# Performance work log

Measured on AMD Instinct MI355X. Metric: run time of the kernel, lower is better.

The kernel has to match this reference:

```python
import jax, jax.numpy as jnp
import numpy as np

EMBED_DIM = 1024
NUM_HEADS = 16
HEAD_DIM = EMBED_DIM // NUM_HEADS
SCALE = HEAD_DIM ** -0.5


def setup_inputs() -> dict:
    key = jax.random.key(0)
    ks = jax.random.split(key, 5)
    B, N, C = 4, 2048, EMBED_DIM
    s = C ** -0.5
    return {
        "x": jax.random.normal(ks[0], (B, N, C), dtype=jnp.float32),
        "w_qkv": jax.random.normal(ks[1], (C, 3 * C), dtype=jnp.float32) * s,
        "b_qkv": jnp.zeros((3 * C,), dtype=jnp.float32),
        "w_proj": jax.random.normal(ks[2], (C, C), dtype=jnp.float32) * s,
        "b_proj": jnp.zeros((C,), dtype=jnp.float32),
    }


def reference(x, w_qkv, b_qkv, w_proj, b_proj):
    B, N, C = x.shape
    H, D = NUM_HEADS, HEAD_DIM
    qkv = x @ w_qkv + b_qkv                      # (B, N, 3C)
    qkv = qkv.reshape(B, N, 3, H, D)
    qkv = jnp.transpose(qkv, (2, 0, 3, 1, 4))    # (3, B, H, N, D)
    q, k, v = qkv[0], qkv[1], qkv[2]
    attn = jnp.einsum('bhnd,bhmd->bhnm', q, k) * SCALE
    attn = jax.nn.softmax(attn, axis=-1)
    out = jnp.einsum('bhnm,bhmd->bhnd', attn, v)  # (B, H, N, D)
    out = jnp.transpose(out, (0, 2, 1, 3)).reshape(B, N, C)
    return out @ w_proj + b_proj
```

## Files before the change

### kernel.cpp

```cpp
#include <hip/hip_runtime.h>

typedef __attribute__((ext_vector_type(8))) short short8v;
typedef __attribute__((ext_vector_type(4))) short short4v;
typedef __attribute__((ext_vector_type(4))) float float4v;
typedef __attribute__((ext_vector_type(4))) unsigned short ushort4v;
typedef __attribute__((ext_vector_type(8))) unsigned short ushort8v;

#define GLOBAL_AS __attribute__((address_space(1)))
#define LDS_AS __attribute__((address_space(3)))

__device__ __forceinline__ void async_cp16(const void* g, void* l) {
  __builtin_amdgcn_global_load_lds((const GLOBAL_AS void*)g, (LDS_AS void*)l, 16, 0, 0);
}

__device__ __forceinline__ unsigned short f2bf(float f) {
  unsigned u = __float_as_uint(f);
  u += 0x7fffu + ((u >> 16) & 1u);
  return (unsigned short)(u >> 16);
}

#if defined(__HIP_DEVICE_COMPILE__)
#if __has_builtin(__builtin_amdgcn_exp2f)
#define EXP2F(x) __builtin_amdgcn_exp2f(x)
#else
#define EXP2F(x) exp2f(x)
#endif
#else
#define EXP2F(x) exp2f(x)
#endif

#if defined(__HIP_DEVICE_COMPILE__) && __has_builtin(__builtin_amdgcn_cvt_pk_bf16_f32)
typedef __attribute__((ext_vector_type(2))) __bf16 bf16x2v;
__device__ __forceinline__ unsigned pk_bf16(float a, float b) {
  bf16x2v r = __builtin_amdgcn_cvt_pk_bf16_f32(a, b);
  return __builtin_bit_cast(unsigned, r);
}
#else
__device__ __forceinline__ unsigned pk_bf16(float a, float b) {
  return (unsigned)f2bf(a) | ((unsigned)f2bf(b) << 16);
}
#endif

#define MFMA_QK(a, b, c) __builtin_amdgcn_mfma_f32_16x16x32_bf16(a, b, c, 0, 0, 0)


__global__ __launch_bounds__(256) void cvt_f32_bf16(const float* __restrict__ src,
                                                    unsigned short* __restrict__ dst) {
  int i = blockIdx.x * 256 + threadIdx.x;
  float4 v = ((const float4*)src)[i];
  ushort4v o;
  o.x = f2bf(v.x); o.y = f2bf(v.y); o.z = f2bf(v.z); o.w = f2bf(v.w);
  ((ushort4v*)dst)[i] = o;
}

__global__ __launch_bounds__(256) void transpose_w(const float* __restrict__ src,
                                                   unsigned short* __restrict__ dst,
                                                   int K, int N) {
  __shared__ float tile[64][65];
  int k0 = blockIdx.x * 64, n0 = blockIdx.y * 64;
  int t = threadIdx.x;
  int tc = t & 15, tr = t >> 4;
#pragma unroll
  for (int p = 0; p < 4; p++) {
    int r = tr + p * 16;
    float4 v = *(const float4*)(src + (size_t)(k0 + r) * N + n0 + tc * 4);
    tile[r][tc * 4 + 0] = v.x; tile[r][tc * 4 + 1] = v.y;
    tile[r][tc * 4 + 2] = v.z; tile[r][tc * 4 + 3] = v.w;
  }
  __syncthreads();
#pragma unroll
  for (int p = 0; p < 4; p++) {
    int rn = tr + p * 16;
    ushort4v o;
    o.x = f2bf(tile[tc * 4 + 0][rn]);
    o.y = f2bf(tile[tc * 4 + 1][rn]);
    o.z = f2bf(tile[tc * 4 + 2][rn]);
    o.w = f2bf(tile[tc * 4 + 3][rn]);
    *(ushort4v*)(dst + (size_t)(n0 + rn) * K + k0 + tc * 4) = o;
  }
}


__global__ __launch_bounds__(256) void gemm_qkv(const unsigned short* __restrict__ A,
                                                const unsigned short* __restrict__ BT,
                                                const float* __restrict__ bias,
                                                unsigned short* __restrict__ Qo,
                                                unsigned short* __restrict__ Ko,
                                                unsigned short* __restrict__ VTo) {
  __shared__ unsigned short As[128 * 32];
  __shared__ unsigned short Bs[128 * 32];
  int tid = threadIdx.x;
  int lane = tid & 63, w = tid >> 6, g = lane >> 4, c = lane & 15;
  int m0 = blockIdx.x * 128, n0 = blockIdx.y * 128;
  int wm = (w & 1) * 64, wn = (w >> 1) * 64;
  float4v acc[4][4] = {};

  for (int k0 = 0; k0 < 1024; k0 += 32) {
    __syncthreads();
#pragma unroll
    for (int p = 0; p < 2; p++) {
      int idx = p * 256 + tid;
      int row = idx >> 2, c8 = (idx & 3) * 8;
      async_cp16(A + (size_t)(m0 + row) * 1024 + k0 + c8, &As[idx * 8]);
      async_cp16(BT + (size_t)(n0 + row) * 1024 + k0 + c8, &Bs[idx * 8]);
    }
    __syncthreads();
    short8v af[4], bf[4];
#pragma unroll
    for (int i = 0; i < 4; i++)
      af[i] = *(const short8v*)(&As[(wm + i * 16 + c) * 32 + g * 8]);
#pragma unroll
    for (int j = 0; j < 4; j++)
      bf[j] = *(const short8v*)(&Bs[(wn + j * 16 + c) * 32 + g * 8]);
#pragma unroll
    for (int i = 0; i < 4; i++)
#pragma unroll
      for (int j = 0; j < 4; j++)
        acc[i][j] = MFMA_QK(af[i], bf[j], acc[i][j]);
  }

  int which = n0 >> 10;
#pragma unroll
  for (int j = 0; j < 4; j++) {
    int ng = n0 + wn + j * 16 + c;
    float bv = bias[ng];
    int h = (ng & 1023) >> 6, d = ng & 63;
#pragma unroll
    for (int i = 0; i < 4; i++) {
#pragma unroll
      for (int r = 0; r < 4; r++) {
        int mg = m0 + wm + i * 16 + g * 4 + r;
        int b = mg >> 11, n = mg & 2047;
        float v = acc[i][j][r] + bv;
        if (which == 0)
          Qo[((size_t)(b * 16 + h) * 2048 + n) * 64 + d] = f2bf(v * 0.18033688011112042f);
        else if (which == 1)
          Ko[((size_t)(b * 16 + h) * 2048 + n) * 64 + d] = f2bf(v);
        else {
          int np = (n & ~31) | (((n >> 2) & 3) << 3) | (((n >> 4) & 1) << 2) | (n & 3);
          VTo[((size_t)(b * 16 + h) * 64 + d) * 2048 + np] = f2bf(v);
        }
      }
    }
  }
}


#define NTOK 2048
#define BK 64

__global__ __launch_bounds__(256, 2) void attn_kernel(const unsigned short* __restrict__ Qg,
                                                      const unsigned short* __restrict__ Kg,
                                                      const unsigned short* __restrict__ VTg,
                                                      unsigned short* __restrict__ Og) {
  __shared__ unsigned short Ks[2][BK * 64];
  __shared__ unsigned short VTs[2][64 * BK];

  int tid = threadIdx.x;
  int lane = tid & 63, w = tid >> 6, g = lane >> 4, c = lane & 15;
  int id = blockIdx.x;
  int xcd = id & 7, within = id >> 3;
  int bh = xcd * 8 + (within >> 3);
  int q0 = (within & 7) * 256;

  const unsigned short* Qb = Qg + (size_t)bh * NTOK * 64;
  const unsigned short* Kb = Kg + (size_t)bh * NTOK * 64;
  const unsigned short* VTb = VTg + (size_t)bh * 64 * NTOK;

  short8v qf[4][2];
#pragma unroll
  for (int nt = 0; nt < 4; nt++)
#pragma unroll
    for (int kk = 0; kk < 2; kk++)
      qf[nt][kk] = *(const short8v*)(Qb + (size_t)(q0 + w * 64 + nt * 16 + c) * 64 +
                                     kk * 32 + g * 8);

  short8v ones8;
#pragma unroll
  for (int i = 0; i < 8; i++) ones8[i] = (short)0x3F80;

  float4v lacc[4] = {};
  float4v o[4][4] = {};

#pragma unroll
  for (int p = 0; p < 2; p++) {
    int idx = p * 256 + tid;
    int row = idx >> 3, ch = idx & 7;
    async_cp16(Kb + (size_t)row * 64 + ((ch ^ (row & 7)) * 8), &Ks[0][idx * 8]);
    async_cp16(VTb + (size_t)row * NTOK + ((ch ^ (row & 7)) * 8), &VTs[0][idx * 8]);
  }

  for (int it = 0; it < NTOK / BK; it++) {
    int pb = it & 1;
    __syncthreads();

    if (it + 1 < NTOK / BK) {
      int kt = (it + 1) * BK;
#pragma unroll
      for (int p = 0; p < 2; p++) {
        int idx = p * 256 + tid;
        int row = idx >> 3, ch = idx & 7;
        async_cp16(Kb + (size_t)(kt + row) * 64 + ((ch ^ (row & 7)) * 8),
                   &Ks[1 - pb][idx * 8]);
        async_cp16(VTb + (size_t)row * NTOK + kt + ((ch ^ (row & 7)) * 8),
                   &VTs[1 - pb][idx * 8]);
      }
    }

    const unsigned short* Kp = &Ks[pb][0];
    const unsigned short* Vp = &VTs[pb][0];

#pragma unroll
    for (int t = 0; t < 2; t++) {
      float4v st[2][4] = {};
      __builtin_amdgcn_s_setprio(1);
#pragma unroll
      for (int mth = 0; mth < 2; mth++) {
        int row = (t * 2 + mth) * 16 + c;
        short8v kf[2];
#pragma unroll
        for (int kk = 0; kk < 2; kk++) {
          int ch = (kk * 4 + g) ^ (row & 7);
          kf[kk] = *(const short8v*)(Kp + row * 64 + ch * 8);
        }
#pragma unroll
        for (int nt = 0; nt < 4; nt++)
#pragma unroll
          for (int kk = 0; kk < 2; kk++)
            st[mth][nt] = MFMA_QK(kf[kk], qf[nt][kk], st[mth][nt]);
      }
      __builtin_amdgcn_s_setprio(0);

      short8v pa8[4];
#pragma unroll
      for (int nt = 0; nt < 4; nt++) {
        float4v a = st[0][nt], b2 = st[1][nt];
        a.x = EXP2F(a.x); a.y = EXP2F(a.y); a.z = EXP2F(a.z); a.w = EXP2F(a.w);
        b2.x = EXP2F(b2.x); b2.y = EXP2F(b2.y); b2.z = EXP2F(b2.z); b2.w = EXP2F(b2.w);
        union { unsigned u[4]; short8v s; } cv;
        cv.u[0] = pk_bf16(a.x, a.y);
        cv.u[1] = pk_bf16(a.z, a.w);
        cv.u[2] = pk_bf16(b2.x, b2.y);
        cv.u[3] = pk_bf16(b2.z, b2.w);
        pa8[nt] = cv.s;
      }

      __builtin_amdgcn_s_setprio(1);
#pragma unroll
      for (int nt_o = 0; nt_o < 4; nt_o++) {
        int d = nt_o * 16 + c;
        int s = (t * 4 + g) ^ (d & 7);
        short8v vb8 = *(const short8v*)(Vp + d * BK + s * 8);
#pragma unroll
        for (int mt = 0; mt < 4; mt++)
          o[mt][nt_o] = MFMA_QK(pa8[mt], vb8, o[mt][nt_o]);
      }
#pragma unroll
      for (int mt = 0; mt < 4; mt++)
        lacc[mt] = MFMA_QK(pa8[mt], ones8, lacc[mt]);
      __builtin_amdgcn_s_setprio(0);
    }
  }

  int b = bh >> 4, h = bh & 15;
#pragma unroll
  for (int mt = 0; mt < 4; mt++) {
    float4v li;
#pragma unroll
    for (int r = 0; r < 4; r++) li[r] = 1.0f / lacc[mt][r];
#pragma unroll
    for (int nt_o = 0; nt_o < 4; nt_o++) {
      float4v v = o[mt][nt_o] * li;
      int col = h * 64 + nt_o * 16 + c;
      int rowbase = b * NTOK + q0 + w * 64 + mt * 16 + g * 4;
#pragma unroll
      for (int r = 0; r < 4; r++)
        Og[(size_t)(rowbase + r) * 1024 + col] = f2bf(v[r]);
    }
  }
}

__global__ __launch_bounds__(256) void gemm_proj(const unsigned short* __restrict__ A,
                                                 const unsigned short* __restrict__ BT,
                                                 const float* __restrict__ bias,
                                                 float* __restrict__ out) {
  __shared__ unsigned short As[128 * 32];
  __shared__ unsigned short Bs[128 * 32];
  int tid = threadIdx.x;
  int lane = tid & 63, w = tid >> 6, g = lane >> 4, c = lane & 15;
  int m0 = blockIdx.x * 128, n0 = blockIdx.y * 128;
  int wm = (w & 1) * 64, wn = (w >> 1) * 64;
  float4v acc[4][4] = {};

  for (int k0 = 0; k0 < 1024; k0 += 32) {
    __syncthreads();
#pragma unroll
    for (int p = 0; p < 2; p++) {
      int idx = p * 256 + tid;
      int row = idx >> 2, c8 = (idx & 3) * 8;
      async_cp16(A + (size_t)(m0 + row) * 1024 + k0 + c8, &As[idx * 8]);
      async_cp16(BT + (size_t)(n0 + row) * 1024 + k0 + c8, &Bs[idx * 8]);
    }
    __syncthreads();
    short8v af[4], bf[4];
#pragma unroll
    for (int i = 0; i < 4; i++)
      af[i] = *(const short8v*)(&As[(wm + i * 16 + c) * 32 + g * 8]);
#pragma unroll
    for (int j = 0; j < 4; j++)
      bf[j] = *(const short8v*)(&Bs[(wn + j * 16 + c) * 32 + g * 8]);
#pragma unroll
    for (int i = 0; i < 4; i++)
#pragma unroll
      for (int j = 0; j < 4; j++)
        acc[i][j] = MFMA_QK(af[i], bf[j], acc[i][j]);
  }

#pragma unroll
  for (int j = 0; j < 4; j++) {
    int ng = n0 + wn + j * 16 + c;
    float bv = bias[ng];
#pragma unroll
    for (int i = 0; i < 4; i++) {
#pragma unroll
      for (int r = 0; r < 4; r++) {
        int mg = m0 + wm + i * 16 + g * 4 + r;
        out[(size_t)mg * 1024 + ng] = acc[i][j][r] + bv;
      }
    }
  }
}


extern "C" void kernel_launch(void* const* d_in, const int* in_sizes, int n_in,
                              void* d_out, int out_size, void* d_ws, size_t ws_size,
                              hipStream_t stream) {
  (void)in_sizes; (void)n_in; (void)out_size; (void)ws_size;
  const float* x = (const float*)d_in[0];
  const float* w_qkv = (const float*)d_in[1];
  const float* b_qkv = (const float*)d_in[2];
  const float* w_proj = (const float*)d_in[3];
  const float* b_proj = (const float*)d_in[4];
  float* out = (float*)d_out;

  unsigned short* x_bf = (unsigned short*)d_ws;
  unsigned short* wqkvT = x_bf + (size_t)8192 * 1024;
  unsigned short* wprojT = wqkvT + (size_t)3072 * 1024;
  unsigned short* qws = wprojT + (size_t)1024 * 1024;
  unsigned short* kws = qws + (size_t)8388608;
  unsigned short* vtws = kws + (size_t)8388608;
  unsigned short* aws = vtws + (size_t)8388608;

  cvt_f32_bf16<<<8192, 256, 0, stream>>>(x, x_bf);
  transpose_w<<<dim3(16, 48), 256, 0, stream>>>(w_qkv, wqkvT, 1024, 3072);
  transpose_w<<<dim3(16, 16), 256, 0, stream>>>(w_proj, wprojT, 1024, 1024);
  gemm_qkv<<<dim3(64, 24), 256, 0, stream>>>(x_bf, wqkvT, b_qkv, qws, kws, vtws);
  attn_kernel<<<512, 256, 0, stream>>>(qws, kws, vtws, aws);
  gemm_proj<<<dim3(64, 8), 256, 0, stream>>>(aws, wprojT, b_proj, out);
}
```

Baseline: 294.9 us.

## Double-buffer LDS tiles with XOR swizzle in QKV and projection GEMMs

Both GEMM kernels now keep two LDS buffers. The async global-to-LDS copy for the next K-slice is issued before the MFMA work on the current slice, which drops the second barrier per iteration and overlaps load latency with compute. The 16-byte chunk placement in LDS is XOR-swizzled by row to reduce bank conflicts on the short8 fragment reads. Launch bounds now request 4 blocks per CU, which doubles LDS per block and may constrain register allocation.

```diff
diff --git a/kernel.cpp b/kernel.cpp
--- a/kernel.cpp
+++ b/kernel.cpp
@@ -81,37 +81,54 @@
 }
 
 
-__global__ __launch_bounds__(256) void gemm_qkv(const unsigned short* __restrict__ A,
-                                                const unsigned short* __restrict__ BT,
-                                                const float* __restrict__ bias,
-                                                unsigned short* __restrict__ Qo,
-                                                unsigned short* __restrict__ Ko,
-                                                unsigned short* __restrict__ VTo) {
-  __shared__ unsigned short As[128 * 32];
-  __shared__ unsigned short Bs[128 * 32];
+__device__ __forceinline__ void stage128x32(const unsigned short* __restrict__ A,
+                                            const unsigned short* __restrict__ BT,
+                                            unsigned short* as, unsigned short* bs,
+                                            int m0, int n0, int k0, int tid) {
+#pragma unroll
+  for (int p = 0; p < 2; p++) {
+    int idx = p * 256 + tid;
+    int row = idx >> 2, s = idx & 3;
+    int ch = s ^ ((row >> 1) & 3);
+    async_cp16(A + (size_t)(m0 + row) * 1024 + k0 + ch * 8, as + idx * 8);
+    async_cp16(BT + (size_t)(n0 + row) * 1024 + k0 + ch * 8, bs + idx * 8);
+  }
+}
+
+
+__global__ __launch_bounds__(256, 4) void gemm_qkv(const unsigned short* __restrict__ A,
+                                                   const unsigned short* __restrict__ BT,
+                                                   const float* __restrict__ bias,
+                                                   unsigned short* __restrict__ Qo,
+                                                   unsigned short* __restrict__ Ko,
+                                                   unsigned short* __restrict__ VTo) {
+  __shared__ unsigned short As[2][128 * 32];
+  __shared__ unsigned short Bs[2][128 * 32];
   int tid = threadIdx.x;
   int lane = tid & 63, w = tid >> 6, g = lane >> 4, c = lane & 15;
   int m0 = blockIdx.x * 128, n0 = blockIdx.y * 128;
   int wm = (w & 1) * 64, wn = (w >> 1) * 64;
   float4v acc[4][4] = {};
 
-  for (int k0 = 0; k0 < 1024; k0 += 32) {
+  stage128x32(A, BT, &As[0][0], &Bs[0][0], m0, n0, 0, tid);
+
+  for (int it = 0; it < 32; ++it) {
+    int pb = it & 1;
     __syncthreads();
-#pragma unroll
-    for (int p = 0; p < 2; p++) {
-      int idx = p * 256 + tid;
-      int row = idx >> 2, c8 = (idx & 3) * 8;
-      async_cp16(A + (size_t)(m0 + row) * 1024 + k0 + c8, &As[idx * 8]);
-      async_cp16(BT + (size_t)(n0 + row) * 1024 + k0 + c8, &Bs[idx * 8]);
-    }
-    __syncthreads();
+    if (it + 1 < 32)
+      stage128x32(A, BT, &As[1 - pb][0], &Bs[1 - pb][0], m0, n0, (it + 1) * 32, tid);
+
     short8v af[4], bf[4];
 #pragma unroll
-    for (int i = 0; i < 4; i++)
-      af[i] = *(const short8v*)(&As[(wm + i * 16 + c) * 32 + g * 8]);
-#pragma unroll
-    for (int j = 0; j < 4; j++)
-      bf[j] = *(const short8v*)(&Bs[(wn + j * 16 + c) * 32 + g * 8]);
+    for (int i = 0; i < 4; i++) {
+      int r = wm + i * 16 + c;
+      af[i] = *(const short8v*)(&As[pb][r * 32 + (g ^ ((r >> 1) & 3)) * 8]);
+    }
+#pragma unroll
+    for (int j = 0; j < 4; j++) {
+      int r = wn + j * 16 + c;
+      bf[j] = *(const short8v*)(&Bs[pb][r * 32 + (g ^ ((r >> 1) & 3)) * 8]);
+    }
 #pragma unroll
     for (int i = 0; i < 4; i++)
 #pragma unroll
@@ -280,35 +297,37 @@
   }
 }
 
-__global__ __launch_bounds__(256) void gemm_proj(const unsigned short* __restrict__ A,
-                                                 const unsigned short* __restrict__ BT,
-                                                 const float* __restrict__ bias,
-                                                 float* __restrict__ out) {
-  __shared__ unsigned short As[128 * 32];
-  __shared__ unsigned short Bs[128 * 32];
+__global__ __launch_bounds__(256, 4) void gemm_proj(const unsigned short* __restrict__ A,
+                                                    const unsigned short* __restrict__ BT,
+                                                    const float* __restrict__ bias,
+                                                    float* __restrict__ out) {
+  __shared__ unsigned short As[2][128 * 32];
+  __shared__ unsigned short Bs[2][128 * 32];
   int tid = threadIdx.x;
   int lane = tid & 63, w = tid >> 6, g = lane >> 4, c = lane & 15;
   int m0 = blockIdx.x * 128, n0 = blockIdx.y * 128;
   int wm = (w & 1) * 64, wn = (w >> 1) * 64;
   float4v acc[4][4] = {};
 
-  for (int k0 = 0; k0 < 1024; k0 += 32) {
+  stage128x32(A, BT, &As[0][0], &Bs[0][0], m0, n0, 0, tid);
+
+  for (int it = 0; it < 32; ++it) {
+    int pb = it & 1;
     __syncthreads();
-#pragma unroll
-    for (int p = 0; p < 2; p++) {
-      int idx = p * 256 + tid;
-      int row = idx >> 2, c8 = (idx & 3) * 8;
-      async_cp16(A + (size_t)(m0 + row) * 1024 + k0 + c8, &As[idx * 8]);
-      async_cp16(BT + (size_t)(n0 + row) * 1024 + k0 + c8, &Bs[idx * 8]);
-    }
-    __syncthreads();
+    if (it + 1 < 32)
+      stage128x32(A, BT, &As[1 - pb][0], &Bs[1 - pb][0], m0, n0, (it + 1) * 32, tid);
+
     short8v af[4], bf[4];
 #pragma unroll
-    for (int i = 0; i < 4; i++)
-      af[i] = *(const short8v*)(&As[(wm + i * 16 + c) * 32 + g * 8]);
-#pragma unroll
-    for (int j = 0; j < 4; j++)
-      bf[j] = *(const short8v*)(&Bs[(wn + j * 16 + c) * 32 + g * 8]);
+    for (int i = 0; i < 4; i++) {
+      int r = wm + i * 16 + c;
+      af[i] = *(const short8v*)(&As[pb][r * 32 + (g ^ ((r >> 1) & 3)) * 8]);
+    }
+#pragma unroll
+    for (int j = 0; j < 4; j++) {
+      int r = wn + j * 16 + c;
+      bf[j] = *(const short8v*)(&Bs[pb][r * 32 + (g ^ ((r >> 1) & 3)) * 8]);
+    }
 #pragma unroll
     for (int i = 0; i < 4; i++)
 #pragma unroll
```

Result: faster. 287.9 us (-2.4%).

## Rewrite QKV and projection GEMMs with larger tiles and triple-buffered async pipeline

Applied to the files above, without the earlier changes.

Both GEMMs now use 512-thread blocks with larger tiles (256x256 for QKV, 128x256 for projection). K-slices are triple-buffered through LDS with async global-to-LDS copies issued two steps ahead and gated by explicit vmcnt waits and raw barriers. LDS chunks are XOR-swizzled to avoid bank conflicts, MFMA phases are wrapped in s_setprio, and block IDs are remapped for L2 locality. This aims to hide global load latency and raise data reuse, in exchange for higher register and LDS pressure and fragile hand-written wait counts.

```diff
diff --git a/kernel.cpp b/kernel.cpp
--- a/kernel.cpp
+++ b/kernel.cpp
@@ -43,6 +43,12 @@
 
 #define MFMA_QK(a, b, c) __builtin_amdgcn_mfma_f32_16x16x32_bf16(a, b, c, 0, 0, 0)
 
+__device__ __forceinline__ void wg_barrier() {
+  asm volatile("" ::: "memory");
+  __builtin_amdgcn_s_barrier();
+  asm volatile("" ::: "memory");
+}
+
 
 __global__ __launch_bounds__(256) void cvt_f32_bf16(const float* __restrict__ src,
                                                     unsigned short* __restrict__ dst) {
@@ -81,55 +87,110 @@
 }
 
 
-__global__ __launch_bounds__(256) void gemm_qkv(const unsigned short* __restrict__ A,
-                                                const unsigned short* __restrict__ BT,
-                                                const float* __restrict__ bias,
-                                                unsigned short* __restrict__ Qo,
-                                                unsigned short* __restrict__ Ko,
-                                                unsigned short* __restrict__ VTo) {
-  __shared__ unsigned short As[128 * 32];
-  __shared__ unsigned short Bs[128 * 32];
+__device__ __forceinline__ void stage256x32(const unsigned short* __restrict__ src,
+                                            unsigned short* dst, int r0, int k0, int tid) {
+#pragma unroll
+  for (int p = 0; p < 2; p++) {
+    int idx = p * 512 + tid;
+    int row = idx >> 2, s = idx & 3;
+    int ch = s ^ ((row >> 1) & 3);
+    async_cp16(src + (size_t)(r0 + row) * 1024 + k0 + ch * 8, dst + idx * 8);
+  }
+}
+
+__device__ __forceinline__ void stage128x32(const unsigned short* __restrict__ src,
+                                            unsigned short* dst, int r0, int k0, int tid) {
+  int row = tid >> 2, s = tid & 3;
+  int ch = s ^ ((row >> 1) & 3);
+  async_cp16(src + (size_t)(r0 + row) * 1024 + k0 + ch * 8, dst + tid * 8);
+}
+
+
+__global__ __launch_bounds__(512, 2) void gemm_qkv(const unsigned short* __restrict__ A,
+                                                   const unsigned short* __restrict__ BT,
+                                                   const float* __restrict__ bias,
+                                                   unsigned short* __restrict__ Qo,
+                                                   unsigned short* __restrict__ Ko,
+                                                   unsigned short* __restrict__ VTo) {
+  __shared__ unsigned short As[3][256 * 32];
+  __shared__ unsigned short Bs[3][256 * 32];
   int tid = threadIdx.x;
-  int lane = tid & 63, w = tid >> 6, g = lane >> 4, c = lane & 15;
-  int m0 = blockIdx.x * 128, n0 = blockIdx.y * 128;
-  int wm = (w & 1) * 64, wn = (w >> 1) * 64;
-  float4v acc[4][4] = {};
-
-  for (int k0 = 0; k0 < 1024; k0 += 32) {
-    __syncthreads();
-#pragma unroll
-    for (int p = 0; p < 2; p++) {
-      int idx = p * 256 + tid;
-      int row = idx >> 2, c8 = (idx & 3) * 8;
-      async_cp16(A + (size_t)(m0 + row) * 1024 + k0 + c8, &As[idx * 8]);
-      async_cp16(BT + (size_t)(n0 + row) * 1024 + k0 + c8, &Bs[idx * 8]);
-    }
-    __syncthreads();
-    short8v af[4], bf[4];
-#pragma unroll
-    for (int i = 0; i < 4; i++)
-      af[i] = *(const short8v*)(&As[(wm + i * 16 + c) * 32 + g * 8]);
-#pragma unroll
-    for (int j = 0; j < 4; j++)
-      bf[j] = *(const short8v*)(&Bs[(wn + j * 16 + c) * 32 + g * 8]);
+  int lane = tid & 63, w = tid >> 6, g = (lane >> 4) & 3, c = lane & 15;
+  int wr = w >> 2, wc = w & 3;
+  int id = blockIdx.x;
+  int swz = (id & 7) * 48 + (id >> 3);
+  int m0 = (swz & 31) * 256, n0 = (swz >> 5) * 256;
+
+  float4v acc[8][4] = {};
+  short8v bf[4];
+
+  stage256x32(A, &As[0][0], m0, 0, tid);
+  stage256x32(BT, &Bs[0][0], n0, 0, tid);
+  stage256x32(A, &As[1][0], m0, 32, tid);
+  stage256x32(BT, &Bs[1][0], n0, 32, tid);
+  asm volatile("s_waitcnt vmcnt(4)" ::: "memory");
+  wg_barrier();
+
+  int cb = 0;
+  for (int t = 0; t < 32; ++t) {
+    int nb = cb + 2; if (nb >= 3) nb -= 3;
+    const unsigned short* Ap = &As[cb][0];
+    const unsigned short* Bp = &Bs[cb][0];
+
+    short8v af[4];
+#pragma unroll
+    for (int i = 0; i < 4; i++) {
+      int r = wr * 128 + i * 16 + c;
+      af[i] = *(const short8v*)(Ap + r * 32 + (g ^ ((r >> 1) & 3)) * 8);
+    }
+#pragma unroll
+    for (int j = 0; j < 4; j++) {
+      int r = wc * 64 + j * 16 + c;
+      bf[j] = *(const short8v*)(Bp + r * 32 + (g ^ ((r >> 1) & 3)) * 8);
+    }
+    if (t + 2 < 32) stage256x32(A, &As[nb][0], m0, (t + 2) * 32, tid);
+    wg_barrier();
+    __builtin_amdgcn_s_setprio(1);
 #pragma unroll
     for (int i = 0; i < 4; i++)
 #pragma unroll
       for (int j = 0; j < 4; j++)
         acc[i][j] = MFMA_QK(af[i], bf[j], acc[i][j]);
+    __builtin_amdgcn_s_setprio(0);
+    wg_barrier();
+
+#pragma unroll
+    for (int i = 0; i < 4; i++) {
+      int r = wr * 128 + 64 + i * 16 + c;
+      af[i] = *(const short8v*)(Ap + r * 32 + (g ^ ((r >> 1) & 3)) * 8);
+    }
+    if (t + 2 < 32) stage256x32(BT, &Bs[nb][0], n0, (t + 2) * 32, tid);
+    if (t < 30) { asm volatile("s_waitcnt vmcnt(4)" ::: "memory"); }
+    else        { asm volatile("s_waitcnt vmcnt(0)" ::: "memory"); }
+    wg_barrier();
+    __builtin_amdgcn_s_setprio(1);
+#pragma unroll
+    for (int i = 0; i < 4; i++)
+#pragma unroll
+      for (int j = 0; j < 4; j++)
+        acc[4 + i][j] = MFMA_QK(af[i], bf[j], acc[4 + i][j]);
+    __builtin_amdgcn_s_setprio(0);
+    wg_barrier();
+
+    cb = cb + 1 == 3 ? 0 : cb + 1;
   }
 
   int which = n0 >> 10;
 #pragma unroll
   for (int j = 0; j < 4; j++) {
-    int ng = n0 + wn + j * 16 + c;
+    int ng = n0 + wc * 64 + j * 16 + c;
     float bv = bias[ng];
     int h = (ng & 1023) >> 6, d = ng & 63;
 #pragma unroll
-    for (int i = 0; i < 4; i++) {
+    for (int i = 0; i < 8; i++) {
 #pragma unroll
       for (int r = 0; r < 4; r++) {
-        int mg = m0 + wm + i * 16 + g * 4 + r;
+        int mg = m0 + wr * 128 + i * 16 + g * 4 + r;
         int b = mg >> 11, n = mg & 2047;
         float v = acc[i][j][r] + bv;
         if (which == 0)
@@ -280,51 +341,88 @@
   }
 }
 
-__global__ __launch_bounds__(256) void gemm_proj(const unsigned short* __restrict__ A,
-                                                 const unsigned short* __restrict__ BT,
-                                                 const float* __restrict__ bias,
-                                                 float* __restrict__ out) {
-  __shared__ unsigned short As[128 * 32];
-  __shared__ unsigned short Bs[128 * 32];
+
+__global__ __launch_bounds__(512, 2) void gemm_proj(const unsigned short* __restrict__ A,
+                                                    const unsigned short* __restrict__ BT,
+                                                    const float* __restrict__ bias,
+                                                    float* __restrict__ out) {
+  __shared__ unsigned short As[3][128 * 32];
+  __shared__ unsigned short Bs[3][256 * 32];
   int tid = threadIdx.x;
-  int lane = tid & 63, w = tid >> 6, g = lane >> 4, c = lane & 15;
-  int m0 = blockIdx.x * 128, n0 = blockIdx.y * 128;
-  int wm = (w & 1) * 64, wn = (w >> 1) * 64;
+  int lane = tid & 63, w = tid >> 6, g = (lane >> 4) & 3, c = lane & 15;
+  int wr = w >> 2, wc = w & 3;
+  int id = blockIdx.x;
+  int swz = (id & 7) * 32 + (id >> 3);
+  int m0 = (swz & 63) * 128, n0 = (swz >> 6) * 256;
+
   float4v acc[4][4] = {};
-
-  for (int k0 = 0; k0 < 1024; k0 += 32) {
-    __syncthreads();
-#pragma unroll
-    for (int p = 0; p < 2; p++) {
-      int idx = p * 256 + tid;
-      int row = idx >> 2, c8 = (idx & 3) * 8;
-      async_cp16(A + (size_t)(m0 + row) * 1024 + k0 + c8, &As[idx * 8]);
-      async_cp16(BT + (size_t)(n0 + row) * 1024 + k0 + c8, &Bs[idx * 8]);
-    }
-    __syncthreads();
-    short8v af[4], bf[4];
-#pragma unroll
-    for (int i = 0; i < 4; i++)
-      af[i] = *(const short8v*)(&As[(wm + i * 16 + c) * 32 + g * 8]);
-#pragma unroll
-    for (int j = 0; j < 4; j++)
-      bf[j] = *(const short8v*)(&Bs[(wn + j * 16 + c) * 32 + g * 8]);
-#pragma unroll
-    for (int i = 0; i < 4; i++)
+  short8v bf[4];
+
+  stage128x32(A, &As[0][0], m0, 0, tid);
+  stage256x32(BT, &Bs[0][0], n0, 0, tid);
+  stage128x32(A, &As[1][0], m0, 32, tid);
+  stage256x32(BT, &Bs[1][0], n0, 32, tid);
+  asm volatile("s_waitcnt vmcnt(3)" ::: "memory");
+  wg_barrier();
+
+  int cb = 0;
+  for (int t = 0; t < 32; ++t) {
+    int nb = cb + 2; if (nb >= 3) nb -= 3;
+    const unsigned short* Ap = &As[cb][0];
+    const unsigned short* Bp = &Bs[cb][0];
+
+    short8v af[2];
+#pragma unroll
+    for (int i = 0; i < 2; i++) {
+      int r = wr * 64 + i * 16 + c;
+      af[i] = *(const short8v*)(Ap + r * 32 + (g ^ ((r >> 1) & 3)) * 8);
+    }
+#pragma unroll
+    for (int j = 0; j < 4; j++) {
+      int r = wc * 64 + j * 16 + c;
+      bf[j] = *(const short8v*)(Bp + r * 32 + (g ^ ((r >> 1) & 3)) * 8);
+    }
+    if (t + 2 < 32) stage128x32(A, &As[nb][0], m0, (t + 2) * 32, tid);
+    wg_barrier();
+    __builtin_amdgcn_s_setprio(1);
+#pragma unroll
+    for (int i = 0; i < 2; i++)
 #pragma unroll
       for (int j = 0; j < 4; j++)
         acc[i][j] = MFMA_QK(af[i], bf[j], acc[i][j]);
+    __builtin_amdgcn_s_setprio(0);
+    wg_barrier();
+
+#pragma unroll
+    for (int i = 0; i < 2; i++) {
+      int r = wr * 64 + 32 + i * 16 + c;
+      af[i] = *(const short8v*)(Ap + r * 32 + (g ^ ((r >> 1) & 3)) * 8);
+    }
+    if (t + 2 < 32) stage256x32(BT, &Bs[nb][0], n0, (t + 2) * 32, tid);
+    if (t < 30) { asm volatile("s_waitcnt vmcnt(3)" ::: "memory"); }
+    else        { asm volatile("s_waitcnt vmcnt(0)" ::: "memory"); }
+    wg_barrier();
+    __builtin_amdgcn_s_setprio(1);
+#pragma unroll
+    for (int i = 0; i < 2; i++)
+#pragma unroll
+      for (int j = 0; j < 4; j++)
+        acc[2 + i][j] = MFMA_QK(af[i], bf[j], acc[2 + i][j]);
+    __builtin_amdgcn_s_setprio(0);
+    wg_barrier();
+
+    cb = cb + 1 == 3 ? 0 : cb + 1;
   }
 
 #pragma unroll
   for (int j = 0; j < 4; j++) {
-    int ng = n0 + wn + j * 16 + c;
+    int ng = n0 + wc * 64 + j * 16 + c;
     float bv = bias[ng];
 #pragma unroll
     for (int i = 0; i < 4; i++) {
 #pragma unroll
       for (int r = 0; r < 4; r++) {
-        int mg = m0 + wm + i * 16 + g * 4 + r;
+        int mg = m0 + wr * 64 + i * 16 + g * 4 + r;
         out[(size_t)mg * 1024 + ng] = acc[i][j][r] + bv;
       }
     }
@@ -354,7 +452,7 @@
   cvt_f32_bf16<<<8192, 256, 0, stream>>>(x, x_bf);
   transpose_w<<<dim3(16, 48), 256, 0, stream>>>(w_qkv, wqkvT, 1024, 3072);
   transpose_w<<<dim3(16, 16), 256, 0, stream>>>(w_proj, wprojT, 1024, 1024);
-  gemm_qkv<<<dim3(64, 24), 256, 0, stream>>>(x_bf, wqkvT, b_qkv, qws, kws, vtws);
+  gemm_qkv<<<384, 512, 0, stream>>>(x_bf, wqkvT, b_qkv, qws, kws, vtws);
   attn_kernel<<<512, 256, 0, stream>>>(qws, kws, vtws, aws);
-  gemm_proj<<<dim3(64, 8), 256, 0, stream>>>(aws, wprojT, b_proj, out);
-}
+  gemm_proj<<<256, 512, 0, stream>>>(aws, wprojT, b_proj, out);
+}
```

New measurement: 336.6 us. 14.1% more time.

## Swizzle GEMM LDS tiles and stage V-transpose epilogue through LDS

Applied to the files above, without the earlier changes.

Applies an XOR swizzle on the 16-byte chunk index when staging A/B tiles into LDS in both the QKV and projection GEMMs, so the per-lane short8 fragment reads hit fewer bank conflicts. For the V third of the QKV GEMM, the epilogue now writes packed bf16 results into a padded LDS tile and reads them back so each lane stores 16-byte vectors along the token dimension, replacing scattered 2-byte transposed writes. This adds an extra shared-memory buffer and two barriers in the V path. It relies on a pk_bf16 helper defined outside the shown code and on the permuted token ordering matching what the attention kernel expects.

```diff
diff --git a/kernel.cpp b/kernel.cpp
--- a/kernel.cpp
+++ b/kernel.cpp
@@ -80,6 +80,19 @@
   }
 }
 
+__device__ __forceinline__ void stage128x32(const unsigned short* __restrict__ src,
+                                            unsigned short* dst, int r0, int k0, int tid) {
+#pragma unroll
+  for (int p = 0; p < 2; p++) {
+    int idx = p * 256 + tid;
+    int row = idx >> 2, s = idx & 3;
+    int ch = s ^ ((row >> 1) & 3);
+    async_cp16(src + (size_t)(r0 + row) * 1024 + k0 + ch * 8, dst + idx * 8);
+  }
+}
+
+
+#define TT_STRIDE 136
 
 __global__ __launch_bounds__(256) void gemm_qkv(const unsigned short* __restrict__ A,
                                                 const unsigned short* __restrict__ BT,
@@ -87,8 +100,9 @@
                                                 unsigned short* __restrict__ Qo,
                                                 unsigned short* __restrict__ Ko,
                                                 unsigned short* __restrict__ VTo) {
-  __shared__ unsigned short As[128 * 32];
-  __shared__ unsigned short Bs[128 * 32];
+  __shared__ unsigned short smem[128 * TT_STRIDE];
+  unsigned short* As = smem;
+  unsigned short* Bs = smem + 4096;
   int tid = threadIdx.x;
   int lane = tid & 63, w = tid >> 6, g = lane >> 4, c = lane & 15;
   int m0 = blockIdx.x * 128, n0 = blockIdx.y * 128;
@@ -97,21 +111,20 @@
 
   for (int k0 = 0; k0 < 1024; k0 += 32) {
     __syncthreads();
-#pragma unroll
-    for (int p = 0; p < 2; p++) {
-      int idx = p * 256 + tid;
-      int row = idx >> 2, c8 = (idx & 3) * 8;
-      async_cp16(A + (size_t)(m0 + row) * 1024 + k0 + c8, &As[idx * 8]);
-      async_cp16(BT + (size_t)(n0 + row) * 1024 + k0 + c8, &Bs[idx * 8]);
-    }
+    stage128x32(A, As, m0, k0, tid);
+    stage128x32(BT, Bs, n0, k0, tid);
     __syncthreads();
     short8v af[4], bf[4];
 #pragma unroll
-    for (int i = 0; i < 4; i++)
-      af[i] = *(const short8v*)(&As[(wm + i * 16 + c) * 32 + g * 8]);
-#pragma unroll
-    for (int j = 0; j < 4; j++)
-      bf[j] = *(const short8v*)(&Bs[(wn + j * 16 + c) * 32 + g * 8]);
+    for (int i = 0; i < 4; i++) {
+      int r = wm + i * 16 + c;
+      af[i] = *(const short8v*)(&As[r * 32 + (g ^ ((r >> 1) & 3)) * 8]);
+    }
+#pragma unroll
+    for (int j = 0; j < 4; j++) {
+      int r = wn + j * 16 + c;
+      bf[j] = *(const short8v*)(&Bs[r * 32 + (g ^ ((r >> 1) & 3)) * 8]);
+    }
 #pragma unroll
     for (int i = 0; i < 4; i++)
 #pragma unroll
@@ -120,27 +133,56 @@
   }
 
   int which = n0 >> 10;
-#pragma unroll
-  for (int j = 0; j < 4; j++) {
-    int ng = n0 + wn + j * 16 + c;
-    float bv = bias[ng];
-    int h = (ng & 1023) >> 6, d = ng & 63;
-#pragma unroll
-    for (int i = 0; i < 4; i++) {
-#pragma unroll
-      for (int r = 0; r < 4; r++) {
-        int mg = m0 + wm + i * 16 + g * 4 + r;
-        int b = mg >> 11, n = mg & 2047;
-        float v = acc[i][j][r] + bv;
-        if (which == 0)
-          Qo[((size_t)(b * 16 + h) * 2048 + n) * 64 + d] = f2bf(v * 0.18033688011112042f);
-        else if (which == 1)
-          Ko[((size_t)(b * 16 + h) * 2048 + n) * 64 + d] = f2bf(v);
-        else {
-          int np = (n & ~31) | (((n >> 2) & 3) << 3) | (((n >> 4) & 1) << 2) | (n & 3);
-          VTo[((size_t)(b * 16 + h) * 64 + d) * 2048 + np] = f2bf(v);
+  if (which != 2) {
+#pragma unroll
+    for (int j = 0; j < 4; j++) {
+      int ng = n0 + wn + j * 16 + c;
+      float bv = bias[ng];
+      int h = (ng & 1023) >> 6, d = ng & 63;
+#pragma unroll
+      for (int i = 0; i < 4; i++) {
+#pragma unroll
+        for (int r = 0; r < 4; r++) {
+          int mg = m0 + wm + i * 16 + g * 4 + r;
+          int b = mg >> 11, n = mg & 2047;
+          float v = acc[i][j][r] + bv;
+          if (which == 0)
+            Qo[((size_t)(b * 16 + h) * 2048 + n) * 64 + d] = f2bf(v * 0.18033688011112042f);
+          else
+            Ko[((size_t)(b * 16 + h) * 2048 + n) * 64 + d] = f2bf(v);
         }
       }
+    }
+  } else {
+    __syncthreads();
+#pragma unroll
+    for (int j = 0; j < 4; j++) {
+      int nl = wn + j * 16 + c;
+      float bv = bias[n0 + nl];
+#pragma unroll
+      for (int i = 0; i < 4; i++) {
+        int ml = wm + i * 16 + g * 4;
+        unsigned p0 = pk_bf16(acc[i][j][0] + bv, acc[i][j][1] + bv);
+        unsigned p1 = pk_bf16(acc[i][j][2] + bv, acc[i][j][3] + bv);
+        *(unsigned*)(smem + nl * TT_STRIDE + ml) = p0;
+        *(unsigned*)(smem + nl * TT_STRIDE + ml + 2) = p1;
+      }
+    }
+    __syncthreads();
+    int rr = lane >> 4, tc = lane & 15;
+    int P = tc & 3, g32 = tc >> 2;
+    int b = m0 >> 11, mloc = m0 & 2047;
+    int h0 = (n0 & 1023) >> 6;
+#pragma unroll
+    for (int s = 0; s < 8; s++) {
+      int row = w * 32 + s * 4 + rr;
+      int h = h0 + (row >> 6), d = row & 63;
+      const unsigned short* bp = smem + row * TT_STRIDE + g32 * 32 + P * 4;
+      union { unsigned long long q[2]; ushort8v v; } u;
+      u.q[0] = *(const unsigned long long*)(bp);
+      u.q[1] = *(const unsigned long long*)(bp + 16);
+      size_t gaddr = ((size_t)(b * 16 + h) * 64 + d) * 2048 + mloc + g32 * 32 + P * 8;
+      *(ushort8v*)(VTo + gaddr) = u.v;
     }
   }
 }
@@ -294,21 +336,20 @@
 
   for (int k0 = 0; k0 < 1024; k0 += 32) {
     __syncthreads();
-#pragma unroll
-    for (int p = 0; p < 2; p++) {
-      int idx = p * 256 + tid;
-      int row = idx >> 2, c8 = (idx & 3) * 8;
-      async_cp16(A + (size_t)(m0 + row) * 1024 + k0 + c8, &As[idx * 8]);
-      async_cp16(BT + (size_t)(n0 + row) * 1024 + k0 + c8, &Bs[idx * 8]);
-    }
+    stage128x32(A, As, m0, k0, tid);
+    stage128x32(BT, Bs, n0, k0, tid);
     __syncthreads();
     short8v af[4], bf[4];
 #pragma unroll
-    for (int i = 0; i < 4; i++)
-      af[i] = *(const short8v*)(&As[(wm + i * 16 + c) * 32 + g * 8]);
-#pragma unroll
-    for (int j = 0; j < 4; j++)
-      bf[j] = *(const short8v*)(&Bs[(wn + j * 16 + c) * 32 + g * 8]);
+    for (int i = 0; i < 4; i++) {
+      int r = wm + i * 16 + c;
+      af[i] = *(const short8v*)(&As[r * 32 + (g ^ ((r >> 1) & 3)) * 8]);
+    }
+#pragma unroll
+    for (int j = 0; j < 4; j++) {
+      int r = wn + j * 16 + c;
+      bf[j] = *(const short8v*)(&Bs[r * 32 + (g ^ ((r >> 1) & 3)) * 8]);
+    }
 #pragma unroll
     for (int i = 0; i < 4; i++)
 #pragma unroll
```

Result: faster. 276.9 us (-6.1%).
